# Kernel optimization log

Measured on AMD Instinct MI355X. Metric: run time of the kernel, lower is better.

The kernel has to match this reference:

```python
import jax, jax.numpy as jnp
import numpy as np

OUT = 12                # out_size (cubic grid)
V = OUT * OUT * OUT     # voxels per roi


def setup_inputs() -> dict:
    key = jax.random.key(0)
    k1, k2, k3, k4, k5 = jax.random.split(key, 5)
    N, P, C = 64, 100000, 16
    # rois: (cx, cy, cz_bottom, dx, dy, dz, rz) with sensible LiDAR-scale boxes
    centers = (jax.random.uniform(k1, (N, 3)) - 0.5) * 16.0
    sizes = jax.random.uniform(k2, (N, 3)) * 3.0 + 1.0
    rz = jax.random.uniform(k3, (N, 1)) * np.float32(np.pi)
    rois = jnp.concatenate([centers, sizes, rz], axis=1)
    pts = jax.random.normal(k4, (P, 3)) * 6.0
    pts_feature = jax.random.normal(k5, (P, C))
    return {"rois": rois, "pts": pts, "pts_feature": pts_feature, "mode": 0}


def _pool_one(roi, pts, pts_feature, mode):
    P, C = pts_feature.shape
    cx, cy, cz, dx, dy, dz, rz = roi
    cz = cz + dz * 0.5                      # bottom center -> box center
    sx = pts[:, 0] - cx
    sy = pts[:, 1] - cy
    lz = pts[:, 2] - cz
    cosa = jnp.cos(-rz)
    sina = jnp.sin(-rz)
    lx = sx * cosa - sy * sina              # rotate into roi frame (by -rz)
    ly = sx * sina + sy * cosa
    inbox = (jnp.abs(lz) <= dz * 0.5) & (jnp.abs(lx) < dx * 0.5) & (jnp.abs(ly) < dy * 0.5)
    xi = jnp.clip(jnp.floor((lx + dx * 0.5) / (dx / OUT)).astype(jnp.int32), 0, OUT - 1)
    yi = jnp.clip(jnp.floor((ly + dy * 0.5) / (dy / OUT)).astype(jnp.int32), 0, OUT - 1)
    zi = jnp.clip(jnp.floor((lz + dz * 0.5) / (dz / OUT)).astype(jnp.int32), 0, OUT - 1)
    vid = (xi * OUT + yi) * OUT + zi        # flat voxel id
    seg = jnp.where(inbox, vid, V)          # out-of-box points -> dump segment V
    cnt = jax.ops.segment_sum(jnp.ones((P,), pts_feature.dtype), seg, num_segments=V + 1)[:V]
    if mode == 0:  # max pool: empty voxels stay 0 (as in CUDA kernel init)
        sm = jax.ops.segment_max(pts_feature, seg, num_segments=V + 1)[:V]
        out = jnp.where(cnt[:, None] > 0, sm, jnp.zeros_like(sm))
    else:          # avg pool
        ss = jax.ops.segment_sum(pts_feature, seg, num_segments=V + 1)[:V]
        out = ss / jnp.maximum(cnt[:, None], 1.0)
    return out.reshape(OUT, OUT, OUT, C)


def reference(rois, pts, pts_feature, mode):
    # [N, OUT, OUT, OUT, C]
    return jax.vmap(lambda r: _pool_one(r, pts, pts_feature, mode))(rois)
```

## Files before the change

kernel.cpp:

```cpp
#include <hip/hip_runtime.h>
#include <hip/hip_bf16.h>

#define OUTDIM 12
#define VOX (OUTDIM * OUTDIM * OUTDIM)
#define CS 4
#define BLOCK 512
#define MAXN 256

__device__ __forceinline__ unsigned enc_f32(float f) {
    unsigned u = __float_as_uint(f);
    return (u & 0x80000000u) ? ~u : (u | 0x80000000u);
}
__device__ __forceinline__ float dec_f32(unsigned e) {
    unsigned u = (e & 0x80000000u) ? (e ^ 0x80000000u) : ~e;
    return __uint_as_float(u);
}
__device__ __forceinline__ float bfu2f(unsigned lo16) {
    return __uint_as_float(lo16 << 16);
}
__device__ __forceinline__ unsigned f2bf_bits(float v) {
    __hip_bfloat16 b = __float2bfloat16(v);
    return (unsigned)__builtin_bit_cast(unsigned short, b);
}

__device__ __forceinline__ bool detect_f32(const void* rois_v, int N) {
    const float* rf = (const float*)rois_v;
    int ndet = N / 2; if (ndet > 8) ndet = 8; if (ndet < 1) ndet = 1;
    bool is_f32 = true;
    for (int i = 0; i < ndet; ++i) {
        float a = rf[i * 7 + 3], b = rf[i * 7 + 4], c = rf[i * 7 + 5];
        is_f32 = is_f32 && (a >= 0.99f) && (a <= 4.01f)
                        && (b >= 0.99f) && (b <= 4.01f)
                        && (c >= 0.99f) && (c <= 4.01f);
    }
    return is_f32;
}

__device__ __forceinline__ int decode_mode(const unsigned* mode_p) {
    int mode = 0;
    if (mode_p != nullptr) {
        unsigned u = *mode_p;
        if (u == 1u || u == 0x3f800000u || (u & 0xffffu) == 0x3f80u) mode = 1;
    }
    return mode;
}

struct RoiParams {
    float cx, cy, cz, cosa, sina, hdx, hdy, hdz, stepx, stepy, stepz;
};

__device__ __forceinline__ RoiParams load_roi(const void* rois_v, int n, bool is_f32) {
    float cx, cy, cz, dx, dy, dz, rz;
    if (is_f32) {
        const float* r = (const float*)rois_v + n * 7;
        cx = r[0]; cy = r[1]; cz = r[2];
        dx = r[3]; dy = r[4]; dz = r[5]; rz = r[6];
    } else {
        const ushort* r = (const ushort*)rois_v + n * 7;
        cx = bfu2f(r[0]); cy = bfu2f(r[1]); cz = bfu2f(r[2]);
        dx = bfu2f(r[3]); dy = bfu2f(r[4]); dz = bfu2f(r[5]); rz = bfu2f(r[6]);
    }
    RoiParams rp;
    rp.cx = cx; rp.cy = cy;
    rp.cz = __fadd_rn(cz, __fmul_rn(dz, 0.5f));
    rp.cosa = cosf(-rz);
    rp.sina = sinf(-rz);
    rp.hdx = __fmul_rn(dx, 0.5f);
    rp.hdy = __fmul_rn(dy, 0.5f);
    rp.hdz = __fmul_rn(dz, 0.5f);
    rp.stepx = __fdiv_rn(dx, (float)OUTDIM);
    rp.stepy = __fdiv_rn(dy, (float)OUTDIM);
    rp.stepz = __fdiv_rn(dz, (float)OUTDIM);
    return rp;
}

__device__ __forceinline__ int voxel_of(const RoiParams& rp, float x, float y, float z) {
    float sx = __fsub_rn(x, rp.cx);
    float sy = __fsub_rn(y, rp.cy);
    float lz = __fsub_rn(z, rp.cz);
    float lx = __fsub_rn(__fmul_rn(sx, rp.cosa), __fmul_rn(sy, rp.sina));
    float ly = __fadd_rn(__fmul_rn(sx, rp.sina), __fmul_rn(sy, rp.cosa));
    bool inbox = (fabsf(lz) <= rp.hdz) && (fabsf(lx) < rp.hdx) && (fabsf(ly) < rp.hdy);
    if (!inbox) return -1;
    int xi = (int)floorf(__fdiv_rn(__fadd_rn(lx, rp.hdx), rp.stepx));
    int yi = (int)floorf(__fdiv_rn(__fadd_rn(ly, rp.hdy), rp.stepy));
    int zi = (int)floorf(__fdiv_rn(__fadd_rn(lz, rp.hdz), rp.stepz));
    xi = min(max(xi, 0), OUTDIM - 1);
    yi = min(max(yi, 0), OUTDIM - 1);
    zi = min(max(zi, 0), OUTDIM - 1);
    return (xi * OUTDIM + yi) * OUTDIM + zi;
}

__global__ void __launch_bounds__(64)
roiaware_scatter3(const void* __restrict__ rois_v,
                  const void* __restrict__ pts_v,
                  const void* __restrict__ feat_v,
                  const unsigned* __restrict__ mode_p,
                  unsigned* __restrict__ acc,
                  unsigned* __restrict__ cnt,
                  int P, int N) {
    __shared__ float4 s_rp[MAXN][3];
    const int lane = threadIdx.x;

    const bool is_f32 = detect_f32(rois_v, N);
    const int mode = decode_mode(mode_p);

    for (int i = lane; i < N; i += 64) {
        RoiParams rp = load_roi(rois_v, i, is_f32);
        s_rp[i][0] = make_float4(rp.cx, rp.cy, rp.cz, rp.cosa);
        s_rp[i][1] = make_float4(rp.sina, rp.hdx, rp.hdy, rp.hdz);
        s_rp[i][2] = make_float4(rp.stepx, rp.stepy, rp.stepz, 0.0f);
    }
    __syncthreads();

    const int p = blockIdx.x * 64 + lane;
    const bool valid = p < P;

    float x = 1e30f, y = 1e30f, z = 1e30f;
    unsigned vals[16];
    #pragma unroll
    for (int c = 0; c < 16; ++c) vals[c] = 0u;

    if (valid) {
        if (is_f32) {
            const float* pf = (const float*)pts_v + (size_t)p * 3;
            x = pf[0]; y = pf[1]; z = pf[2];
            const float* f = (const float*)feat_v + (size_t)p * 16;
            #pragma unroll
            for (int c = 0; c < 16; ++c) {
                float v = f[c];
                vals[c] = (mode == 0) ? enc_f32(v) : __float_as_uint(v);
            }
        } else {
            const ushort* pu = (const ushort*)pts_v + (size_t)p * 3;
            x = bfu2f(pu[0]); y = bfu2f(pu[1]); z = bfu2f(pu[2]);
            const ushort* f = (const ushort*)feat_v + (size_t)p * 16;
            uint4 w0 = *(const uint4*)f;
            uint4 w1 = *(const uint4*)(f + 8);
            unsigned w[8] = {w0.x, w0.y, w0.z, w0.w, w1.x, w1.y, w1.z, w1.w};
            #pragma unroll
            for (int k = 0; k < 8; ++k) {
                float v0 = bfu2f(w[k] & 0xffffu);
                float v1 = __uint_as_float(w[k] & 0xffff0000u);
                vals[2 * k]     = (mode == 0) ? enc_f32(v0) : __float_as_uint(v0);
                vals[2 * k + 1] = (mode == 0) ? enc_f32(v1) : __float_as_uint(v1);
            }
        }
    }

    for (int n = 0; n < N; ++n) {
        float4 ra = s_rp[n][0];
        float4 rb = s_rp[n][1];
        float4 rc = s_rp[n][2];

        float sx = __fsub_rn(x, ra.x);
        float sy = __fsub_rn(y, ra.y);
        float lz = __fsub_rn(z, ra.z);
        float lx = __fsub_rn(__fmul_rn(sx, ra.w), __fmul_rn(sy, rb.x));
        float ly = __fadd_rn(__fmul_rn(sx, rb.x), __fmul_rn(sy, ra.w));
        bool inbox = (fabsf(lz) <= rb.w) && (fabsf(lx) < rb.y) && (fabsf(ly) < rb.z);
        if (!inbox) continue;

        int xi = (int)floorf(__fdiv_rn(__fadd_rn(lx, rb.y), rc.x));
        int yi = (int)floorf(__fdiv_rn(__fadd_rn(ly, rb.z), rc.y));
        int zi = (int)floorf(__fdiv_rn(__fadd_rn(lz, rb.w), rc.z));
        xi = min(max(xi, 0), OUTDIM - 1);
        yi = min(max(yi, 0), OUTDIM - 1);
        zi = min(max(zi, 0), OUTDIM - 1);
        int vid = (xi * OUTDIM + yi) * OUTDIM + zi;

        size_t vbase = (size_t)n * VOX + vid;
        unsigned* a = acc + vbase * 16;
        if (mode == 0) {
            #pragma unroll
            for (int c = 0; c < 16; ++c) atomicMax(&a[c], vals[c]);
        } else {
            atomicAdd(&cnt[vbase], 1u);
            #pragma unroll
            for (int c = 0; c < 16; ++c)
                atomicAdd((float*)&a[c], __uint_as_float(vals[c]));
        }
    }
}

__global__ void __launch_bounds__(256)
roiaware_finalize3(const void* __restrict__ rois_v,
                   const unsigned* __restrict__ acc,
                   const unsigned* __restrict__ cnt,
                   const unsigned* __restrict__ mode_p,
                   void* __restrict__ out_v,
                   int total_pairs, int N) {
    int i = blockIdx.x * blockDim.x + threadIdx.x;
    if (i >= total_pairs) return;
    const bool is_f32 = detect_f32(rois_v, N);
    const int mode = decode_mode(mode_p);

    uint2 a = *(const uint2*)(acc + (size_t)i * 2);
    float v0, v1;
    if (mode == 0) {
        v0 = a.x ? dec_f32(a.x) : 0.0f;
        v1 = a.y ? dec_f32(a.y) : 0.0f;
    } else {
        unsigned c = cnt[i >> 3];
        float inv = 1.0f / fmaxf((float)c, 1.0f);
        v0 = __uint_as_float(a.x) * inv;
        v1 = __uint_as_float(a.y) * inv;
    }
    if (is_f32) {
        ((float2*)out_v)[i] = make_float2(v0, v1);
    } else {
        ((unsigned*)out_v)[i] = f2bf_bits(v0) | (f2bf_bits(v1) << 16);
    }
}

__global__ void __launch_bounds__(BLOCK)
roiaware_pool(const void* __restrict__ rois_v,
              const void* __restrict__ pts_v,
              const void* __restrict__ feat_v,
              const unsigned* __restrict__ mode_p,
              void* __restrict__ out_v,
              int P, int C, int N) {
    __shared__ unsigned s_acc[VOX * CS];
    __shared__ unsigned s_cnt[VOX];

    const int tid = threadIdx.x;
    const int c0  = blockIdx.x * CS;
    const int n   = blockIdx.y;

    for (int i = tid; i < VOX * CS; i += BLOCK) s_acc[i] = 0u;
    for (int i = tid; i < VOX; i += BLOCK) s_cnt[i] = 0u;

    const bool is_f32 = detect_f32(rois_v, N);
    const int mode = decode_mode(mode_p);
    const RoiParams rp = load_roi(rois_v, n, is_f32);

    const float*  pts_f  = (const float*)pts_v;
    const ushort* pts_u  = (const ushort*)pts_v;
    const float*  feat_f = (const float*)feat_v;
    const ushort* feat_u = (const ushort*)feat_v;

    __syncthreads();

    for (int p = tid; p < P; p += BLOCK) {
        float x, y, z;
        if (is_f32) {
            x = pts_f[p * 3 + 0]; y = pts_f[p * 3 + 1]; z = pts_f[p * 3 + 2];
        } else {
            x = bfu2f(pts_u[p * 3 + 0]);
            y = bfu2f(pts_u[p * 3 + 1]);
            z = bfu2f(pts_u[p * 3 + 2]);
        }
        int vid = voxel_of(rp, x, y, z);
        if (vid < 0) continue;

        atomicAdd(&s_cnt[vid], 1u);

        for (int j = 0; j < CS && (c0 + j) < C; ++j) {
            float fv = is_f32 ? feat_f[(size_t)p * C + c0 + j]
                              : bfu2f(feat_u[(size_t)p * C + c0 + j]);
            unsigned* a = &s_acc[vid * CS + j];
            if (mode == 0) atomicMax(a, enc_f32(fv));
            else           atomicAdd((float*)a, fv);
        }
    }

    __syncthreads();

    for (int i = tid; i < VOX * CS; i += BLOCK) {
        int v = i / CS;
        int j = i % CS;
        if (c0 + j >= C) continue;
        unsigned c = s_cnt[v];
        float val;
        if (mode == 0) {
            val = (c > 0) ? dec_f32(s_acc[i]) : 0.0f;
        } else {
            val = __uint_as_float(s_acc[i]) / fmaxf((float)c, 1.0f);
        }
        size_t oi = ((size_t)n * VOX + v) * C + c0 + j;
        if (is_f32) ((float*)out_v)[oi] = val;
        else        ((__hip_bfloat16*)out_v)[oi] = __float2bfloat16(val);
    }
}

extern "C" void kernel_launch(void* const* d_in, const int* in_sizes, int n_in,
                              void* d_out, int out_size, void* d_ws, size_t ws_size,
                              hipStream_t stream) {
    const void* rois = d_in[0];
    const void* pts  = d_in[1];
    const void* feat = d_in[2];
    const unsigned* mode_p = nullptr;
    if (n_in >= 4 && in_sizes[3] >= 1 && d_in[3] != nullptr) {
        mode_p = (const unsigned*)d_in[3];
    }

    int N = in_sizes[0] / 7;
    int P = in_sizes[1] / 3;
    int C = in_sizes[2] / P;

    size_t need = ((size_t)N * VOX * C + (size_t)N * VOX) * sizeof(unsigned);

    if (C == 16 && N <= MAXN && ws_size >= need) {
        unsigned* acc = (unsigned*)d_ws;
        unsigned* cnt = acc + (size_t)N * VOX * 16;
        (void)hipMemsetAsync(d_ws, 0, need, stream);

        int nblocks = (P + 63) / 64;
        roiaware_scatter3<<<nblocks, 64, 0, stream>>>(
            rois, pts, feat, mode_p, acc, cnt, P, N);

        int total_pairs = N * VOX * 8;
        roiaware_finalize3<<<(total_pairs + 255) / 256, 256, 0, stream>>>(
            rois, acc, cnt, mode_p, d_out, total_pairs, N);
    } else {
        dim3 grid((C + CS - 1) / CS, N);
        roiaware_pool<<<grid, BLOCK, 0, stream>>>(rois, pts, feat, mode_p,
                                                  d_out, P, C, N);
    }
}
```

Baseline: 87.88 us.

## Precompute ROI params in prep kernel, add radius precheck, lazy feature loads

```diff
diff --git a/kernel.cpp b/kernel.cpp
--- a/kernel.cpp
+++ b/kernel.cpp
@@ -91,79 +91,74 @@
     return (xi * OUTDIM + yi) * OUTDIM + zi;
 }
 
-__global__ void __launch_bounds__(64)
-roiaware_scatter3(const void* __restrict__ rois_v,
-                  const void* __restrict__ pts_v,
+__global__ void __launch_bounds__(256)
+roiaware_prep4(const void* __restrict__ rois_v,
+               const unsigned* __restrict__ mode_p,
+               float* __restrict__ prm,
+               unsigned* __restrict__ hdr,
+               uint4* __restrict__ zbase,
+               int nz, int N) {
+    int t = blockIdx.x * 256 + threadIdx.x;
+    for (int i = t; i < nz; i += gridDim.x * 256)
+        zbase[i] = make_uint4(0u, 0u, 0u, 0u);
+
+    if (blockIdx.x == 0) {
+        const bool is_f32 = detect_f32(rois_v, N);
+        if (threadIdx.x == 0) {
+            hdr[0] = is_f32 ? 1u : 0u;
+            hdr[1] = (unsigned)decode_mode(mode_p);
+        }
+        if ((int)threadIdx.x < N) {
+            RoiParams rp = load_roi(rois_v, threadIdx.x, is_f32);
+            float r2 = __fmul_rn(rp.hdx * rp.hdx + rp.hdy * rp.hdy, 1.00002f);
+            float* q = prm + (size_t)threadIdx.x * 12;
+            q[0] = rp.cx;   q[1] = rp.cy;   q[2]  = rp.cz;    q[3]  = r2;
+            q[4] = rp.hdz;  q[5] = rp.cosa; q[6]  = rp.sina;  q[7]  = rp.hdx;
+            q[8] = rp.hdy;  q[9] = rp.stepx; q[10] = rp.stepy; q[11] = rp.stepz;
+        }
+    }
+}
+
+__global__ void __launch_bounds__(256)
+roiaware_scatter4(const void* __restrict__ pts_v,
                   const void* __restrict__ feat_v,
-                  const unsigned* __restrict__ mode_p,
+                  const float* __restrict__ prm,
+                  const unsigned* __restrict__ hdr,
                   unsigned* __restrict__ acc,
                   unsigned* __restrict__ cnt,
                   int P, int N) {
-    __shared__ float4 s_rp[MAXN][3];
-    const int lane = threadIdx.x;
-
-    const bool is_f32 = detect_f32(rois_v, N);
-    const int mode = decode_mode(mode_p);
-
-    for (int i = lane; i < N; i += 64) {
-        RoiParams rp = load_roi(rois_v, i, is_f32);
-        s_rp[i][0] = make_float4(rp.cx, rp.cy, rp.cz, rp.cosa);
-        s_rp[i][1] = make_float4(rp.sina, rp.hdx, rp.hdy, rp.hdz);
-        s_rp[i][2] = make_float4(rp.stepx, rp.stepy, rp.stepz, 0.0f);
-    }
-    __syncthreads();
-
-    const int p = blockIdx.x * 64 + lane;
-    const bool valid = p < P;
+    const int p = blockIdx.x * 256 + threadIdx.x;
+    const bool is_f32 = hdr[0] != 0u;
+    const int mode = (int)hdr[1];
 
     float x = 1e30f, y = 1e30f, z = 1e30f;
-    unsigned vals[16];
-    #pragma unroll
-    for (int c = 0; c < 16; ++c) vals[c] = 0u;
-
-    if (valid) {
+    if (p < P) {
         if (is_f32) {
             const float* pf = (const float*)pts_v + (size_t)p * 3;
             x = pf[0]; y = pf[1]; z = pf[2];
-            const float* f = (const float*)feat_v + (size_t)p * 16;
-            #pragma unroll
-            for (int c = 0; c < 16; ++c) {
-                float v = f[c];
-                vals[c] = (mode == 0) ? enc_f32(v) : __float_as_uint(v);
-            }
         } else {
             const ushort* pu = (const ushort*)pts_v + (size_t)p * 3;
             x = bfu2f(pu[0]); y = bfu2f(pu[1]); z = bfu2f(pu[2]);
-            const ushort* f = (const ushort*)feat_v + (size_t)p * 16;
-            uint4 w0 = *(const uint4*)f;
-            uint4 w1 = *(const uint4*)(f + 8);
-            unsigned w[8] = {w0.x, w0.y, w0.z, w0.w, w1.x, w1.y, w1.z, w1.w};
-            #pragma unroll
-            for (int k = 0; k < 8; ++k) {
-                float v0 = bfu2f(w[k] & 0xffffu);
-                float v1 = __uint_as_float(w[k] & 0xffff0000u);
-                vals[2 * k]     = (mode == 0) ? enc_f32(v0) : __float_as_uint(v0);
-                vals[2 * k + 1] = (mode == 0) ? enc_f32(v1) : __float_as_uint(v1);
-            }
-        }
-    }
-
+        }
+    }
+
+    #pragma unroll 4
     for (int n = 0; n < N; ++n) {
-        float4 ra = s_rp[n][0];
-        float4 rb = s_rp[n][1];
-        float4 rc = s_rp[n][2];
-
-        float sx = __fsub_rn(x, ra.x);
-        float sy = __fsub_rn(y, ra.y);
-        float lz = __fsub_rn(z, ra.z);
-        float lx = __fsub_rn(__fmul_rn(sx, ra.w), __fmul_rn(sy, rb.x));
-        float ly = __fadd_rn(__fmul_rn(sx, rb.x), __fmul_rn(sy, ra.w));
-        bool inbox = (fabsf(lz) <= rb.w) && (fabsf(lx) < rb.y) && (fabsf(ly) < rb.z);
-        if (!inbox) continue;
-
-        int xi = (int)floorf(__fdiv_rn(__fadd_rn(lx, rb.y), rc.x));
-        int yi = (int)floorf(__fdiv_rn(__fadd_rn(ly, rb.z), rc.y));
-        int zi = (int)floorf(__fdiv_rn(__fadd_rn(lz, rb.w), rc.z));
+        const float* q = prm + (size_t)n * 12;
+        float sx = __fsub_rn(x, q[0]);
+        float sy = __fsub_rn(y, q[1]);
+        float lz = __fsub_rn(z, q[2]);
+        float d2 = __builtin_fmaf(sy, sy, __fmul_rn(sx, sx));
+        if (!((d2 < q[3]) && (fabsf(lz) <= q[4]))) continue;
+
+        float cosa = q[5], sina = q[6], hdx = q[7], hdy = q[8];
+        float lx = __fsub_rn(__fmul_rn(sx, cosa), __fmul_rn(sy, sina));
+        float ly = __fadd_rn(__fmul_rn(sx, sina), __fmul_rn(sy, cosa));
+        if (!((fabsf(lx) < hdx) && (fabsf(ly) < hdy))) continue;
+
+        int xi = (int)floorf(__fdiv_rn(__fadd_rn(lx, hdx), q[9]));
+        int yi = (int)floorf(__fdiv_rn(__fadd_rn(ly, hdy), q[10]));
+        int zi = (int)floorf(__fdiv_rn(__fadd_rn(lz, q[4]), q[11]));
         xi = min(max(xi, 0), OUTDIM - 1);
         yi = min(max(yi, 0), OUTDIM - 1);
         zi = min(max(zi, 0), OUTDIM - 1);
@@ -171,29 +166,54 @@
 
         size_t vbase = (size_t)n * VOX + vid;
         unsigned* a = acc + vbase * 16;
+
         if (mode == 0) {
-            #pragma unroll
-            for (int c = 0; c < 16; ++c) atomicMax(&a[c], vals[c]);
+            if (is_f32) {
+                const float* f = (const float*)feat_v + (size_t)p * 16;
+                #pragma unroll
+                for (int c = 0; c < 16; ++c) atomicMax(&a[c], enc_f32(f[c]));
+            } else {
+                const ushort* f = (const ushort*)feat_v + (size_t)p * 16;
+                uint4 w0 = *(const uint4*)f;
+                uint4 w1 = *(const uint4*)(f + 8);
+                unsigned w[8] = {w0.x, w0.y, w0.z, w0.w, w1.x, w1.y, w1.z, w1.w};
+                #pragma unroll
+                for (int k = 0; k < 8; ++k) {
+                    atomicMax(&a[2 * k],     enc_f32(bfu2f(w[k] & 0xffffu)));
+                    atomicMax(&a[2 * k + 1], enc_f32(__uint_as_float(w[k] & 0xffff0000u)));
+                }
+            }
         } else {
             atomicAdd(&cnt[vbase], 1u);
-            #pragma unroll
-            for (int c = 0; c < 16; ++c)
-                atomicAdd((float*)&a[c], __uint_as_float(vals[c]));
+            if (is_f32) {
+                const float* f = (const float*)feat_v + (size_t)p * 16;
+                #pragma unroll
+                for (int c = 0; c < 16; ++c) atomicAdd((float*)&a[c], f[c]);
+            } else {
+                const ushort* f = (const ushort*)feat_v + (size_t)p * 16;
+                uint4 w0 = *(const uint4*)f;
+                uint4 w1 = *(const uint4*)(f + 8);
+                unsigned w[8] = {w0.x, w0.y, w0.z, w0.w, w1.x, w1.y, w1.z, w1.w};
+                #pragma unroll
+                for (int k = 0; k < 8; ++k) {
+                    atomicAdd((float*)&a[2 * k],     bfu2f(w[k] & 0xffffu));
+                    atomicAdd((float*)&a[2 * k + 1], __uint_as_float(w[k] & 0xffff0000u));
+                }
+            }
         }
     }
 }
 
 __global__ void __launch_bounds__(256)
-roiaware_finalize3(const void* __restrict__ rois_v,
+roiaware_finalize4(const unsigned* __restrict__ hdr,
                    const unsigned* __restrict__ acc,
                    const unsigned* __restrict__ cnt,
-                   const unsigned* __restrict__ mode_p,
                    void* __restrict__ out_v,
-                   int total_pairs, int N) {
+                   int total_pairs) {
     int i = blockIdx.x * blockDim.x + threadIdx.x;
     if (i >= total_pairs) return;
-    const bool is_f32 = detect_f32(rois_v, N);
-    const int mode = decode_mode(mode_p);
+    const bool is_f32 = hdr[0] != 0u;
+    const int mode = (int)hdr[1];
 
     uint2 a = *(const uint2*)(acc + (size_t)i * 2);
     float v0, v1;
@@ -298,20 +318,25 @@
     int P = in_sizes[1] / 3;
     int C = in_sizes[2] / P;
 
-    size_t need = ((size_t)N * VOX * C + (size_t)N * VOX) * sizeof(unsigned);
+    size_t head_dwords = (size_t)MAXN * 12 + 4;
+    size_t need = (head_dwords + (size_t)N * VOX * 17) * sizeof(unsigned);
 
     if (C == 16 && N <= MAXN && ws_size >= need) {
-        unsigned* acc = (unsigned*)d_ws;
+        float*    prm = (float*)d_ws;
+        unsigned* hdr = (unsigned*)d_ws + (size_t)MAXN * 12;
+        unsigned* acc = hdr + 4;
         unsigned* cnt = acc + (size_t)N * VOX * 16;
-        (void)hipMemsetAsync(d_ws, 0, need, stream);
-
-        int nblocks = (P + 63) / 64;
-        roiaware_scatter3<<<nblocks, 64, 0, stream>>>(
-            rois, pts, feat, mode_p, acc, cnt, P, N);
+
+        int nz = (int)((size_t)N * VOX * 17 / 4);
+        roiaware_prep4<<<1024, 256, 0, stream>>>(
+            rois, mode_p, prm, hdr, (uint4*)acc, nz, N);
+
+        roiaware_scatter4<<<(P + 255) / 256, 256, 0, stream>>>(
+            pts, feat, prm, hdr, acc, cnt, P, N);
 
         int total_pairs = N * VOX * 8;
-        roiaware_finalize3<<<(total_pairs + 255) / 256, 256, 0, stream>>>(
-            rois, acc, cnt, mode_p, d_out, total_pairs, N);
+        roiaware_finalize4<<<(total_pairs + 255) / 256, 256, 0, stream>>>(
+            hdr, acc, cnt, d_out, total_pairs);
     } else {
         dim3 grid((C + CS - 1) / CS, N);
         roiaware_pool<<<grid, BLOCK, 0, stream>>>(rois, pts, feat, mode_p,
```

After: 92.32 us. 1.05x slower.

## Replace global-atomic scatter with per-ROI shared-memory pooling kernel

Applied to the files above, without the earlier changes.

```diff
diff --git a/kernel.cpp b/kernel.cpp
--- a/kernel.cpp
+++ b/kernel.cpp
@@ -5,11 +5,12 @@
 #define VOX (OUTDIM * OUTDIM * OUTDIM)
 #define CS 4
 #define BLOCK 512
-#define MAXN 256
-
+
+__device__ __forceinline__ unsigned enc_bits(unsigned u) {
+    return (u & 0x80000000u) ? ~u : (u | 0x80000000u);
+}
 __device__ __forceinline__ unsigned enc_f32(float f) {
-    unsigned u = __float_as_uint(f);
-    return (u & 0x80000000u) ? ~u : (u | 0x80000000u);
+    return enc_bits(__float_as_uint(f));
 }
 __device__ __forceinline__ float dec_f32(unsigned e) {
     unsigned u = (e & 0x80000000u) ? (e ^ 0x80000000u) : ~e;
@@ -91,125 +92,128 @@
     return (xi * OUTDIM + yi) * OUTDIM + zi;
 }
 
-__global__ void __launch_bounds__(64)
-roiaware_scatter3(const void* __restrict__ rois_v,
-                  const void* __restrict__ pts_v,
-                  const void* __restrict__ feat_v,
-                  const unsigned* __restrict__ mode_p,
-                  unsigned* __restrict__ acc,
-                  unsigned* __restrict__ cnt,
-                  int P, int N) {
-    __shared__ float4 s_rp[MAXN][3];
-    const int lane = threadIdx.x;
-
-    const bool is_f32 = detect_f32(rois_v, N);
-    const int mode = decode_mode(mode_p);
-
-    for (int i = lane; i < N; i += 64) {
-        RoiParams rp = load_roi(rois_v, i, is_f32);
-        s_rp[i][0] = make_float4(rp.cx, rp.cy, rp.cz, rp.cosa);
-        s_rp[i][1] = make_float4(rp.sina, rp.hdx, rp.hdy, rp.hdz);
-        s_rp[i][2] = make_float4(rp.stepx, rp.stepy, rp.stepz, 0.0f);
-    }
-    __syncthreads();
-
-    const int p = blockIdx.x * 64 + lane;
-    const bool valid = p < P;
-
-    float x = 1e30f, y = 1e30f, z = 1e30f;
-    unsigned vals[16];
-    #pragma unroll
-    for (int c = 0; c < 16; ++c) vals[c] = 0u;
-
-    if (valid) {
-        if (is_f32) {
-            const float* pf = (const float*)pts_v + (size_t)p * 3;
-            x = pf[0]; y = pf[1]; z = pf[2];
-            const float* f = (const float*)feat_v + (size_t)p * 16;
+__device__ __forceinline__ void accum_event(unsigned* s_acc, unsigned* s_cnt,
+                                            const void* feat_v, bool is_f32,
+                                            int mode, int p, int vid) {
+    unsigned* a = s_acc + vid * 16;
+    const uint4* f4 = (const uint4*)((const char*)feat_v +
+                                     (size_t)p * (is_f32 ? 64 : 32));
+    if (is_f32) {
+        uint4 w0 = f4[0], w1 = f4[1], w2 = f4[2], w3 = f4[3];
+        unsigned w[16] = {w0.x, w0.y, w0.z, w0.w, w1.x, w1.y, w1.z, w1.w,
+                          w2.x, w2.y, w2.z, w2.w, w3.x, w3.y, w3.z, w3.w};
+        if (mode == 0) {
             #pragma unroll
-            for (int c = 0; c < 16; ++c) {
-                float v = f[c];
-                vals[c] = (mode == 0) ? enc_f32(v) : __float_as_uint(v);
+            for (int c = 0; c < 16; ++c) atomicMax(&a[c], enc_bits(w[c]));
+        } else {
+            atomicAdd(&s_cnt[vid], 1u);
+            #pragma unroll
+            for (int c = 0; c < 16; ++c)
+                atomicAdd((float*)&a[c], __uint_as_float(w[c]));
+        }
+    } else {
+        uint4 w0 = f4[0], w1 = f4[1];
+        unsigned w[8] = {w0.x, w0.y, w0.z, w0.w, w1.x, w1.y, w1.z, w1.w};
+        if (mode == 0) {
+            #pragma unroll
+            for (int k = 0; k < 8; ++k) {
+                atomicMax(&a[2 * k],     enc_bits((w[k] & 0xffffu) << 16));
+                atomicMax(&a[2 * k + 1], enc_bits(w[k] & 0xffff0000u));
             }
         } else {
-            const ushort* pu = (const ushort*)pts_v + (size_t)p * 3;
-            x = bfu2f(pu[0]); y = bfu2f(pu[1]); z = bfu2f(pu[2]);
-            const ushort* f = (const ushort*)feat_v + (size_t)p * 16;
-            uint4 w0 = *(const uint4*)f;
-            uint4 w1 = *(const uint4*)(f + 8);
-            unsigned w[8] = {w0.x, w0.y, w0.z, w0.w, w1.x, w1.y, w1.z, w1.w};
+            atomicAdd(&s_cnt[vid], 1u);
             #pragma unroll
             for (int k = 0; k < 8; ++k) {
-                float v0 = bfu2f(w[k] & 0xffffu);
-                float v1 = __uint_as_float(w[k] & 0xffff0000u);
-                vals[2 * k]     = (mode == 0) ? enc_f32(v0) : __float_as_uint(v0);
-                vals[2 * k + 1] = (mode == 0) ? enc_f32(v1) : __float_as_uint(v1);
+                atomicAdd((float*)&a[2 * k],     bfu2f(w[k] & 0xffffu));
+                atomicAdd((float*)&a[2 * k + 1], __uint_as_float(w[k] & 0xffff0000u));
             }
         }
     }
-
-    for (int n = 0; n < N; ++n) {
-        float4 ra = s_rp[n][0];
-        float4 rb = s_rp[n][1];
-        float4 rc = s_rp[n][2];
-
-        float sx = __fsub_rn(x, ra.x);
-        float sy = __fsub_rn(y, ra.y);
-        float lz = __fsub_rn(z, ra.z);
-        float lx = __fsub_rn(__fmul_rn(sx, ra.w), __fmul_rn(sy, rb.x));
-        float ly = __fadd_rn(__fmul_rn(sx, rb.x), __fmul_rn(sy, ra.w));
-        bool inbox = (fabsf(lz) <= rb.w) && (fabsf(lx) < rb.y) && (fabsf(ly) < rb.z);
-        if (!inbox) continue;
-
-        int xi = (int)floorf(__fdiv_rn(__fadd_rn(lx, rb.y), rc.x));
-        int yi = (int)floorf(__fdiv_rn(__fadd_rn(ly, rb.z), rc.y));
-        int zi = (int)floorf(__fdiv_rn(__fadd_rn(lz, rb.w), rc.z));
-        xi = min(max(xi, 0), OUTDIM - 1);
-        yi = min(max(yi, 0), OUTDIM - 1);
-        zi = min(max(zi, 0), OUTDIM - 1);
-        int vid = (xi * OUTDIM + yi) * OUTDIM + zi;
-
-        size_t vbase = (size_t)n * VOX + vid;
-        unsigned* a = acc + vbase * 16;
-        if (mode == 0) {
-            #pragma unroll
-            for (int c = 0; c < 16; ++c) atomicMax(&a[c], vals[c]);
-        } else {
-            atomicAdd(&cnt[vbase], 1u);
-            #pragma unroll
-            for (int c = 0; c < 16; ++c)
-                atomicAdd((float*)&a[c], __uint_as_float(vals[c]));
-        }
-    }
-}
-
-__global__ void __launch_bounds__(256)
-roiaware_finalize3(const void* __restrict__ rois_v,
-                   const unsigned* __restrict__ acc,
-                   const unsigned* __restrict__ cnt,
-                   const unsigned* __restrict__ mode_p,
-                   void* __restrict__ out_v,
-                   int total_pairs, int N) {
-    int i = blockIdx.x * blockDim.x + threadIdx.x;
-    if (i >= total_pairs) return;
+}
+
+__global__ void __launch_bounds__(512)
+roiaware_pool16(const void* __restrict__ rois_v,
+                const void* __restrict__ pts_v,
+                const void* __restrict__ feat_v,
+                const unsigned* __restrict__ mode_p,
+                void* __restrict__ out_v,
+                int P, int N) {
+    __shared__ unsigned s_acc[VOX * 16];
+    __shared__ unsigned s_cnt[VOX];
+
+    const int tid = threadIdx.x;
+    const int n   = blockIdx.x;
+
     const bool is_f32 = detect_f32(rois_v, N);
-    const int mode = decode_mode(mode_p);
-
-    uint2 a = *(const uint2*)(acc + (size_t)i * 2);
-    float v0, v1;
+    const int  mode   = decode_mode(mode_p);
+    const RoiParams rp = load_roi(rois_v, n, is_f32);
+    const float r2 = __fmul_rn(
+        __fadd_rn(__fmul_rn(rp.hdx, rp.hdx), __fmul_rn(rp.hdy, rp.hdy)),
+        1.00002f);
+
+    for (int i = tid; i < VOX * 16; i += 512) s_acc[i] = 0u;
+    if (mode != 0)
+        for (int i = tid; i < VOX; i += 512) s_cnt[i] = 0u;
+    __syncthreads();
+
+    const float*  pts_f = (const float*)pts_v;
+    const ushort* pts_u = (const ushort*)pts_v;
+
+    for (int p0 = tid; p0 < P; p0 += 2048) {
+        int   pp[4];
+        float xs[4], ys[4], zs[4];
+        #pragma unroll
+        for (int s = 0; s < 4; ++s) {
+            int p = p0 + s * 512;
+            pp[s] = p;
+            if (p < P) {
+                if (is_f32) {
+                    xs[s] = pts_f[p * 3 + 0];
+                    ys[s] = pts_f[p * 3 + 1];
+                    zs[s] = pts_f[p * 3 + 2];
+                } else {
+                    xs[s] = bfu2f(pts_u[p * 3 + 0]);
+                    ys[s] = bfu2f(pts_u[p * 3 + 1]);
+                    zs[s] = bfu2f(pts_u[p * 3 + 2]);
+                }
+            } else {
+                xs[s] = 1e30f; ys[s] = 1e30f; zs[s] = 1e30f;
+            }
+        }
+        #pragma unroll
+        for (int s = 0; s < 4; ++s) {
+            float sx = __fsub_rn(xs[s], rp.cx);
+            float sy = __fsub_rn(ys[s], rp.cy);
+            float lz = __fsub_rn(zs[s], rp.cz);
+            float d2 = __builtin_fmaf(sy, sy, __fmul_rn(sx, sx));
+            if ((d2 < r2) && (fabsf(lz) <= rp.hdz)) {
+                int vid = voxel_of(rp, xs[s], ys[s], zs[s]);
+                if (vid >= 0)
+                    accum_event(s_acc, s_cnt, feat_v, is_f32, mode, pp[s], vid);
+            }
+        }
+    }
+
+    __syncthreads();
+
+    const size_t obase = (size_t)n * (VOX * 8);
     if (mode == 0) {
-        v0 = a.x ? dec_f32(a.x) : 0.0f;
-        v1 = a.y ? dec_f32(a.y) : 0.0f;
+        for (int i = tid; i < VOX * 8; i += 512) {
+            unsigned e0 = s_acc[i * 2], e1 = s_acc[i * 2 + 1];
+            float v0 = e0 ? dec_f32(e0) : 0.0f;
+            float v1 = e1 ? dec_f32(e1) : 0.0f;
+            if (is_f32) ((float2*)out_v)[obase + i] = make_float2(v0, v1);
+            else ((unsigned*)out_v)[obase + i] = f2bf_bits(v0) | (f2bf_bits(v1) << 16);
+        }
     } else {
-        unsigned c = cnt[i >> 3];
-        float inv = 1.0f / fmaxf((float)c, 1.0f);
-        v0 = __uint_as_float(a.x) * inv;
-        v1 = __uint_as_float(a.y) * inv;
-    }
-    if (is_f32) {
-        ((float2*)out_v)[i] = make_float2(v0, v1);
-    } else {
-        ((unsigned*)out_v)[i] = f2bf_bits(v0) | (f2bf_bits(v1) << 16);
+        for (int i = tid; i < VOX * 8; i += 512) {
+            unsigned c = s_cnt[i >> 3];
+            float inv = 1.0f / fmaxf((float)c, 1.0f);
+            float v0 = __uint_as_float(s_acc[i * 2])     * inv;
+            float v1 = __uint_as_float(s_acc[i * 2 + 1]) * inv;
+            if (is_f32) ((float2*)out_v)[obase + i] = make_float2(v0, v1);
+            else ((unsigned*)out_v)[obase + i] = f2bf_bits(v0) | (f2bf_bits(v1) << 16);
+        }
     }
 }
 
@@ -298,20 +302,11 @@
     int P = in_sizes[1] / 3;
     int C = in_sizes[2] / P;
 
-    size_t need = ((size_t)N * VOX * C + (size_t)N * VOX) * sizeof(unsigned);
-
-    if (C == 16 && N <= MAXN && ws_size >= need) {
-        unsigned* acc = (unsigned*)d_ws;
-        unsigned* cnt = acc + (size_t)N * VOX * 16;
-        (void)hipMemsetAsync(d_ws, 0, need, stream);
-
-        int nblocks = (P + 63) / 64;
-        roiaware_scatter3<<<nblocks, 64, 0, stream>>>(
-            rois, pts, feat, mode_p, acc, cnt, P, N);
-
-        int total_pairs = N * VOX * 8;
-        roiaware_finalize3<<<(total_pairs + 255) / 256, 256, 0, stream>>>(
-            rois, acc, cnt, mode_p, d_out, total_pairs, N);
+    (void)d_ws; (void)ws_size;
+
+    if (C == 16 && N > 0) {
+        roiaware_pool16<<<N, 512, 0, stream>>>(rois, pts, feat, mode_p,
+                                               d_out, P, N);
     } else {
         dim3 grid((C + CS - 1) / CS, N);
         roiaware_pool<<<grid, BLOCK, 0, stream>>>(rois, pts, feat, mode_p,
```

Result: slower. 165.4 us (+88.3%).

## Split scatter grid over ROI groups and add bounding-sphere early reject

Applied to the files above, without the earlier changes.

```diff
diff --git a/kernel.cpp b/kernel.cpp
--- a/kernel.cpp
+++ b/kernel.cpp
@@ -6,10 +6,13 @@
 #define CS 4
 #define BLOCK 512
 #define MAXN 256
-
+#define RY 16
+
+__device__ __forceinline__ unsigned enc_bits(unsigned u) {
+    return (u & 0x80000000u) ? ~u : (u | 0x80000000u);
+}
 __device__ __forceinline__ unsigned enc_f32(float f) {
-    unsigned u = __float_as_uint(f);
-    return (u & 0x80000000u) ? ~u : (u | 0x80000000u);
+    return enc_bits(__float_as_uint(f));
 }
 __device__ __forceinline__ float dec_f32(unsigned e) {
     unsigned u = (e & 0x80000000u) ? (e ^ 0x80000000u) : ~e;
@@ -92,84 +95,89 @@
 }
 
 __global__ void __launch_bounds__(64)
-roiaware_scatter3(const void* __restrict__ rois_v,
+roiaware_scatter7(const void* __restrict__ rois_v,
                   const void* __restrict__ pts_v,
                   const void* __restrict__ feat_v,
                   const unsigned* __restrict__ mode_p,
                   unsigned* __restrict__ acc,
                   unsigned* __restrict__ cnt,
                   int P, int N) {
-    __shared__ float4 s_rp[MAXN][3];
+    __shared__ float4 s_rp[RY][3];
     const int lane = threadIdx.x;
+    const int nbase = blockIdx.y * RY;
 
     const bool is_f32 = detect_f32(rois_v, N);
     const int mode = decode_mode(mode_p);
 
-    for (int i = lane; i < N; i += 64) {
-        RoiParams rp = load_roi(rois_v, i, is_f32);
-        s_rp[i][0] = make_float4(rp.cx, rp.cy, rp.cz, rp.cosa);
-        s_rp[i][1] = make_float4(rp.sina, rp.hdx, rp.hdy, rp.hdz);
-        s_rp[i][2] = make_float4(rp.stepx, rp.stepy, rp.stepz, 0.0f);
+    if (lane < RY && (nbase + lane) < N) {
+        RoiParams rp = load_roi(rois_v, nbase + lane, is_f32);
+        float r3 = __fmul_rn(rp.hdx * rp.hdx + rp.hdy * rp.hdy + rp.hdz * rp.hdz,
+                             1.00002f);
+        s_rp[lane][0] = make_float4(rp.cx, rp.cy, rp.cz, r3);
+        s_rp[lane][1] = make_float4(rp.cosa, rp.sina, rp.hdx, rp.hdy);
+        s_rp[lane][2] = make_float4(rp.hdz, rp.stepx, rp.stepy, rp.stepz);
     }
     __syncthreads();
 
     const int p = blockIdx.x * 64 + lane;
-    const bool valid = p < P;
 
     float x = 1e30f, y = 1e30f, z = 1e30f;
     unsigned vals[16];
     #pragma unroll
     for (int c = 0; c < 16; ++c) vals[c] = 0u;
 
-    if (valid) {
+    if (p < P) {
         if (is_f32) {
             const float* pf = (const float*)pts_v + (size_t)p * 3;
             x = pf[0]; y = pf[1]; z = pf[2];
-            const float* f = (const float*)feat_v + (size_t)p * 16;
+            const uint4* f4 = (const uint4*)((const float*)feat_v + (size_t)p * 16);
+            uint4 w0 = f4[0], w1 = f4[1], w2 = f4[2], w3 = f4[3];
+            unsigned w[16] = {w0.x, w0.y, w0.z, w0.w, w1.x, w1.y, w1.z, w1.w,
+                              w2.x, w2.y, w2.z, w2.w, w3.x, w3.y, w3.z, w3.w};
             #pragma unroll
-            for (int c = 0; c < 16; ++c) {
-                float v = f[c];
-                vals[c] = (mode == 0) ? enc_f32(v) : __float_as_uint(v);
-            }
+            for (int c = 0; c < 16; ++c)
+                vals[c] = (mode == 0) ? enc_bits(w[c]) : w[c];
         } else {
             const ushort* pu = (const ushort*)pts_v + (size_t)p * 3;
             x = bfu2f(pu[0]); y = bfu2f(pu[1]); z = bfu2f(pu[2]);
-            const ushort* f = (const ushort*)feat_v + (size_t)p * 16;
-            uint4 w0 = *(const uint4*)f;
-            uint4 w1 = *(const uint4*)(f + 8);
+            const uint4* f4 = (const uint4*)((const ushort*)feat_v + (size_t)p * 16);
+            uint4 w0 = f4[0], w1 = f4[1];
             unsigned w[8] = {w0.x, w0.y, w0.z, w0.w, w1.x, w1.y, w1.z, w1.w};
             #pragma unroll
             for (int k = 0; k < 8; ++k) {
-                float v0 = bfu2f(w[k] & 0xffffu);
-                float v1 = __uint_as_float(w[k] & 0xffff0000u);
-                vals[2 * k]     = (mode == 0) ? enc_f32(v0) : __float_as_uint(v0);
-                vals[2 * k + 1] = (mode == 0) ? enc_f32(v1) : __float_as_uint(v1);
+                unsigned b0 = (w[k] & 0xffffu) << 16;
+                unsigned b1 = w[k] & 0xffff0000u;
+                vals[2 * k]     = (mode == 0) ? enc_bits(b0) : b0;
+                vals[2 * k + 1] = (mode == 0) ? enc_bits(b1) : b1;
             }
         }
     }
 
-    for (int n = 0; n < N; ++n) {
-        float4 ra = s_rp[n][0];
-        float4 rb = s_rp[n][1];
-        float4 rc = s_rp[n][2];
-
-        float sx = __fsub_rn(x, ra.x);
-        float sy = __fsub_rn(y, ra.y);
-        float lz = __fsub_rn(z, ra.z);
-        float lx = __fsub_rn(__fmul_rn(sx, ra.w), __fmul_rn(sy, rb.x));
-        float ly = __fadd_rn(__fmul_rn(sx, rb.x), __fmul_rn(sy, ra.w));
-        bool inbox = (fabsf(lz) <= rb.w) && (fabsf(lx) < rb.y) && (fabsf(ly) < rb.z);
+    const int rmax = min(RY, N - nbase);
+    for (int j = 0; j < rmax; ++j) {
+        float4 q0 = s_rp[j][0];
+        float sx = __fsub_rn(x, q0.x);
+        float sy = __fsub_rn(y, q0.y);
+        float lz = __fsub_rn(z, q0.z);
+        float d3 = __builtin_fmaf(lz, lz, __builtin_fmaf(sy, sy, __fmul_rn(sx, sx)));
+        if (!(d3 < q0.w)) continue;
+
+        float4 q1 = s_rp[j][1];
+        float4 q2 = s_rp[j][2];
+        float lx = __fsub_rn(__fmul_rn(sx, q1.x), __fmul_rn(sy, q1.y));
+        float ly = __fadd_rn(__fmul_rn(sx, q1.y), __fmul_rn(sy, q1.x));
+        bool inbox = (fabsf(lz) <= q2.x) && (fabsf(lx) < q1.z) && (fabsf(ly) < q1.w);
         if (!inbox) continue;
 
-        int xi = (int)floorf(__fdiv_rn(__fadd_rn(lx, rb.y), rc.x));
-        int yi = (int)floorf(__fdiv_rn(__fadd_rn(ly, rb.z), rc.y));
-        int zi = (int)floorf(__fdiv_rn(__fadd_rn(lz, rb.w), rc.z));
+        int xi = (int)floorf(__fdiv_rn(__fadd_rn(lx, q1.z), q2.y));
+        int yi = (int)floorf(__fdiv_rn(__fadd_rn(ly, q1.w), q2.z));
+        int zi = (int)floorf(__fdiv_rn(__fadd_rn(lz, q2.x), q2.w));
         xi = min(max(xi, 0), OUTDIM - 1);
         yi = min(max(yi, 0), OUTDIM - 1);
         zi = min(max(zi, 0), OUTDIM - 1);
         int vid = (xi * OUTDIM + yi) * OUTDIM + zi;
 
-        size_t vbase = (size_t)n * VOX + vid;
+        size_t vbase = (size_t)(nbase + j) * VOX + vid;
         unsigned* a = acc + vbase * 16;
         if (mode == 0) {
             #pragma unroll
@@ -184,7 +192,7 @@
 }
 
 __global__ void __launch_bounds__(256)
-roiaware_finalize3(const void* __restrict__ rois_v,
+roiaware_finalize7(const void* __restrict__ rois_v,
                    const unsigned* __restrict__ acc,
                    const unsigned* __restrict__ cnt,
                    const unsigned* __restrict__ mode_p,
@@ -298,19 +306,19 @@
     int P = in_sizes[1] / 3;
     int C = in_sizes[2] / P;
 
-    size_t need = ((size_t)N * VOX * C + (size_t)N * VOX) * sizeof(unsigned);
+    size_t need = ((size_t)N * VOX * 16 + (size_t)N * VOX) * sizeof(unsigned);
 
     if (C == 16 && N <= MAXN && ws_size >= need) {
         unsigned* acc = (unsigned*)d_ws;
         unsigned* cnt = acc + (size_t)N * VOX * 16;
         (void)hipMemsetAsync(d_ws, 0, need, stream);
 
-        int nblocks = (P + 63) / 64;
-        roiaware_scatter3<<<nblocks, 64, 0, stream>>>(
+        dim3 sg((P + 63) / 64, (N + RY - 1) / RY);
+        roiaware_scatter7<<<sg, 64, 0, stream>>>(
             rois, pts, feat, mode_p, acc, cnt, P, N);
 
         int total_pairs = N * VOX * 8;
-        roiaware_finalize3<<<(total_pairs + 255) / 256, 256, 0, stream>>>(
+        roiaware_finalize7<<<(total_pairs + 255) / 256, 256, 0, stream>>>(
             rois, acc, cnt, mode_p, d_out, total_pairs, N);
     } else {
         dim3 grid((C + CS - 1) / CS, N);
```

New measurement: 91.86 us. 4.5% more time.
